# Kernel tuning notes

Hardware: AMD Instinct MI355X
Metric: run time of the kernel (lower is better)

## Reference

```python
import jax, jax.numpy as jnp
import numpy as np

WS = 8          # window size
HEAD_DIM = 32
C = 128
B, H, W = 8, 256, 256


def _grid_sample(img, grid):
    # torch F.grid_sample, bilinear, padding_mode='zeros', align_corners=True
    # img [N,C,Hi,Wi]; grid [N,Ho,Wo,2] with (x,y) in [-1,1]
    N, Cc, Hi, Wi = img.shape
    gx = (grid[..., 0] + 1.0) * 0.5 * (Wi - 1)
    gy = (grid[..., 1] + 1.0) * 0.5 * (Hi - 1)
    x0 = jnp.floor(gx); y0 = jnp.floor(gy)
    wx1 = gx - x0; wy1 = gy - y0

    def gather(ix, iy):
        valid = ((ix >= 0) & (ix < Wi) & (iy >= 0) & (iy < Hi)).astype(img.dtype)
        ixc = jnp.clip(ix, 0, Wi - 1).astype(jnp.int32)
        iyc = jnp.clip(iy, 0, Hi - 1).astype(jnp.int32)
        v = jax.vmap(lambda im, yy, xx: im[:, yy, xx])(img, iyc, ixc)  # [N,C,Ho,Wo]
        return v * valid[:, None]

    return (gather(x0, y0) * ((1 - wx1) * (1 - wy1))[:, None]
            + gather(x0 + 1, y0) * (wx1 * (1 - wy1))[:, None]
            + gather(x0, y0 + 1) * ((1 - wx1) * wy1)[:, None]
            + gather(x0 + 1, y0 + 1) * (wx1 * wy1)[:, None])


def _rel_bias(rpp):
    cord = np.array([[i, j] for i in range(WS) for j in range(WS)])
    rel = cord[:, None, :] - cord[None, :, :] + WS - 1   # [p2,p2,2]
    return rpp[:, rel[..., 0], rel[..., 1]]               # [h,p2,p2]


def _mask(w1, w2, p, shift):
    s = p - shift
    m = np.zeros((w1, w2, p, p, p, p), dtype=bool)
    m[-1, :, :s, :, s:, :] = True
    m[-1, :, s:, :, :s, :] = True
    m[:, -1, :, :s, :, s:] = True
    m[:, -1, :, s:, :, :s] = True
    return jnp.asarray(m.reshape(1, 1, w1 * w2, p * p, p * p))


def setup_inputs() -> dict:
    key = jax.random.key(0)
    ks = jax.random.split(key, 8)
    s = 0.02
    return {
        'x': jax.random.normal(ks[0], (B, H, W, C), jnp.float32),
        'rpp': jax.random.normal(ks[1], (C // HEAD_DIM, 2 * WS - 1, 2 * WS - 1), jnp.float32) * s,
        'wi_w': jax.random.normal(ks[2], (C, 2), jnp.float32) * s,
        'wi_b': jnp.zeros((2,), jnp.float32),
        'w1_w': jax.random.normal(ks[3], (C, 2), jnp.float32) * s,
        'w1_b': jnp.zeros((2,), jnp.float32),
        'w2_w': jax.random.normal(ks[4], (WS * WS * 2, 2), jnp.float32) * s,
        'w2_b': jnp.zeros((2,), jnp.float32),
        'q_w': jax.random.normal(ks[5], (C, C), jnp.float32) * s,
        'q_b': jnp.zeros((C,), jnp.float32),
        'kv_w': jax.random.normal(ks[6], (C, 2 * C), jnp.float32) * s,
        'kv_b': jnp.zeros((2 * C,), jnp.float32),
        'o_w': jax.random.normal(ks[7], (C, C), jnp.float32) * s,
        'o_b': jnp.zeros((C,), jnp.float32),
    }


def reference(x, rpp, wi_w, wi_b, w1_w, w1_b, w2_w, w2_b, q_w, q_b, kv_w, kv_b, o_w, o_b):
    shift = WS // 2
    b, Hh, Ww, c = x.shape
    w1, w2 = Hh // WS, Ww // WS
    nw, p2 = w1 * w2, WS * WS
    h = c // HEAD_DIM

    # cyclic shift (type != 'W')
    x = jnp.roll(x, (-shift, -shift), axis=(1, 2))
    xw = x.reshape(b, w1, WS, w2, WS, c).transpose(0, 1, 3, 2, 4, 5)  # [b,w1,w2,p,p,c]

    off_intra = xw @ wi_w + wi_b                                       # [b,w1,w2,p,p,2]
    oi = xw @ w1_w + w1_b                                              # [b,w1,w2,p,p,2]
    oi = oi.reshape(b, w1, w2, WS * WS * 2) @ w2_w + w2_b              # [b,w1,w2,2]

    # --- inter-window deformable sampling ---
    gy, gx = np.meshgrid(np.arange(w1), np.arange(w2), indexing='ij')
    gridw = jnp.asarray(np.stack((gx, gy), -1), jnp.float32)           # [w1,w2,2]
    og = gridw[None, :, :, None, None, :] + oi[:, :, :, None, None, :]
    og = jnp.broadcast_to(og, (b, w1, w2, WS, WS, 2))
    og = og / ((max(w1, w2) - 1) / 2) - 1.0
    ximg = xw.transpose(0, 3, 4, 5, 1, 2).reshape(b * p2, c, w1, w2)
    gint = og.transpose(0, 3, 4, 1, 2, 5).reshape(b * p2, w1, w2, 2)
    xd = _grid_sample(ximg, gint)                                      # [b*p2,c,w1,w2]
    xd = xd.reshape(b, WS, WS, c, w1, w2).transpose(0, 4, 5, 1, 2, 3)  # [b,w1,w2,p,p,c]

    # --- intra-window deformable sampling ---
    gy, gx = np.meshgrid(np.arange(WS), np.arange(WS), indexing='ij')
    gridp = jnp.asarray(np.stack((gx, gy), -1), jnp.float32)           # [p,p,2]
    og2 = gridp[None, None] + off_intra.reshape(b, nw, WS, WS, 2)
    og2 = og2 / ((WS - 1) / 2) - 1.0
    xd2 = xd.transpose(0, 1, 2, 5, 3, 4).reshape(b * nw, c, WS, WS)
    g2 = og2.reshape(b * nw, WS, WS, 2)
    xd2 = _grid_sample(xd2, g2).reshape(b, w1, w2, c, WS, WS).transpose(0, 1, 2, 4, 5, 3)

    # --- windowed attention ---
    xq = xw.reshape(b, nw, p2, c)
    xkv = xd2.reshape(b, nw, p2, c)
    q = (xq @ q_w + q_b).reshape(b, nw, p2, h, HEAD_DIM).transpose(3, 0, 1, 2, 4)
    kv = (xkv @ kv_w + kv_b).reshape(b, nw, p2, 2 * h, HEAD_DIM)
    k = kv[..., :h, :].transpose(3, 0, 1, 2, 4)
    v = kv[..., h:, :].transpose(3, 0, 1, 2, 4)

    scale = HEAD_DIM ** (-0.5)
    sim = jnp.einsum('hbwpc,hbwqc->hbwpq', q, k) * scale
    sim = sim + _rel_bias(rpp)[:, None, None]
    sim = jnp.where(_mask(w1, w2, WS, shift), -jnp.inf, sim)
    probs = jax.nn.softmax(sim, axis=-1)
    out = jnp.einsum('hbwpq,hbwqc->hbwpc', probs, v)
    out = out.transpose(1, 2, 3, 0, 4).reshape(b, nw, p2, c)
    out = out @ o_w + o_b
    out = out.reshape(b, w1, w2, WS, WS, c).transpose(0, 1, 3, 2, 4, 5).reshape(b, Hh, Ww, c)
    out = jnp.roll(out, (shift, shift), axis=(1, 2))
    return out
```

## Files before the change

### kernel.cpp

```cpp
#include <hip/hip_runtime.h>
#include <hip/hip_bf16.h>


#define WS_    8
#define SHIFT_ 4
#define C_     128
#define IMG_   256

typedef __attribute__((ext_vector_type(8))) short short8;
typedef __attribute__((ext_vector_type(4))) short short4v;
typedef __attribute__((ext_vector_type(4))) float f32x4;

#define MFMA(a,b,c) __builtin_amdgcn_mfma_f32_16x16x32_bf16((a),(b),(c),0,0,0)

__device__ __forceinline__ short f2bf(float f){
    unsigned u = __float_as_uint(f);
    u = u + 0x7fffu + ((u >> 16) & 1u);
    return (short)(u >> 16);
}
__device__ __forceinline__ float bf2f(short s){
    return __uint_as_float(((unsigned)(unsigned short)s) << 16);
}

__global__ void dgwa_prep(const float* __restrict__ q_w, const float* __restrict__ kv_w,
                          const float* __restrict__ o_w, short* __restrict__ ws){
    int idx = blockIdx.x*256 + threadIdx.x;
    if (idx < 16384){ int co = idx>>7, ci = idx&127; ws[idx] = f2bf(q_w[ci*128 + co]); }
    else if (idx < 49152){ int i = idx-16384; int co = i>>7, ci = i&127; ws[idx] = f2bf(kv_w[ci*256 + co]); }
    else { int i = idx-49152; int co = i>>7, ci = i&127; ws[idx] = f2bf(o_w[ci*128 + co]); }
}

__global__ __launch_bounds__(512, 4)
void dgwa_fused(const float* __restrict__ x, const float* __restrict__ rpp,
                const float* __restrict__ wi_w, const float* __restrict__ wi_b,
                const float* __restrict__ w1_w, const float* __restrict__ w1_b,
                const float* __restrict__ w2_w, const float* __restrict__ w2_b,
                const float* __restrict__ q_b,  const float* __restrict__ kv_b,
                const float* __restrict__ o_b,
                const short* __restrict__ wsw,
                float* __restrict__ out)
{
    __shared__ __align__(16) char smem[75296];
    short* s_xw   = (short*)(smem);
    short* s_xd2  = (short*)(smem + 17408);
    short* s_p    = (short*)(smem + 17408);
    float* s_outT = (float*)(smem + 17408);
    short* s_k    = (short*)(smem + 34816);
    short* s_xd   = (short*)(smem + 34816);
    short* s_vT   = (short*)(smem + 52224);
    float* s_rpp  = (float*)(smem + 70656);
    float* s_off  = (float*)(smem + 74256);
    float* s_red  = (float*)(smem + 74768);
    float* s_oi   = (float*)(smem + 75280);

    const int t   = threadIdx.x;
    const int wv  = t >> 6, l = t & 63, l15 = l & 15, quad = l >> 4;
    const int win = blockIdx.x;
    const int bb  = win >> 10, wy = (win >> 5) & 31, wx = win & 31;
    const f32x4 zf = {0.f, 0.f, 0.f, 0.f};

    const short* qw  = wsw;
    const short* kvw = wsw + 16384;
    const short* ow  = wsw + 49152;

    {
        const int tok = t >> 3, part = t & 7;
        const int i = tok >> 3, j = tok & 7;
        const int grow = (wy*8 + i + SHIFT_) & 255;
        const int gcol = (wx*8 + j + SHIFT_) & 255;
        const float* xr = x + (((size_t)bb*IMG_ + grow)*IMG_ + gcol)*C_ + part*16;
        float di0=0.f, di1=0.f, d10=0.f, d11=0.f;
        #pragma unroll
        for (int c4 = 0; c4 < 4; ++c4){
            const float4 a4 = *(const float4*)(xr + c4*4);
            const int ch = part*16 + c4*4;
            di0 += a4.x*wi_w[ch*2+0]+a4.y*wi_w[ch*2+2]+a4.z*wi_w[ch*2+4]+a4.w*wi_w[ch*2+6];
            di1 += a4.x*wi_w[ch*2+1]+a4.y*wi_w[ch*2+3]+a4.z*wi_w[ch*2+5]+a4.w*wi_w[ch*2+7];
            d10 += a4.x*w1_w[ch*2+0]+a4.y*w1_w[ch*2+2]+a4.z*w1_w[ch*2+4]+a4.w*w1_w[ch*2+6];
            d11 += a4.x*w1_w[ch*2+1]+a4.y*w1_w[ch*2+3]+a4.z*w1_w[ch*2+5]+a4.w*w1_w[ch*2+7];
            short4v sv = { f2bf(a4.x), f2bf(a4.y), f2bf(a4.z), f2bf(a4.w) };
            *(short4v*)&s_xw[tok*136 + part*16 + c4*4] = sv;
        }
        di0 += __shfl_xor(di0,1); di0 += __shfl_xor(di0,2); di0 += __shfl_xor(di0,4);
        di1 += __shfl_xor(di1,1); di1 += __shfl_xor(di1,2); di1 += __shfl_xor(di1,4);
        d10 += __shfl_xor(d10,1); d10 += __shfl_xor(d10,2); d10 += __shfl_xor(d10,4);
        d11 += __shfl_xor(d11,1); d11 += __shfl_xor(d11,2); d11 += __shfl_xor(d11,4);
        if (part == 0){
            s_off[tok*2+0] = di0 + wi_b[0];
            s_off[tok*2+1] = di1 + wi_b[1];
            s_red[tok*2+0] = d10 + w1_b[0];
            s_red[tok*2+1] = d11 + w1_b[1];
        }
    }
    for (int idx = t; idx < 900; idx += 512) s_rpp[idx] = rpp[idx];
    __syncthreads();
    if (t < 64){
        const float a0 = s_red[t*2+0], a1 = s_red[t*2+1];
        float p0 = a0*w2_w[(t*2+0)*2+0] + a1*w2_w[(t*2+1)*2+0];
        float p1 = a0*w2_w[(t*2+0)*2+1] + a1*w2_w[(t*2+1)*2+1];
        #pragma unroll
        for (int m = 1; m < 64; m <<= 1){ p0 += __shfl_xor(p0,m); p1 += __shfl_xor(p1,m); }
        if (t == 0){ s_oi[0] = p0 + w2_b[0]; s_oi[1] = p1 + w2_b[1]; }
    }
    __syncthreads();

    {
        const int tok = t >> 3, part = t & 7;
        const int i = tok >> 3, j = tok & 7;
        const float gx = (float)wx + s_oi[0];
        const float gy = (float)wy + s_oi[1];
        const float fx0 = floorf(gx), fy0 = floorf(gy);
        const int ix0 = (int)fx0, iy0 = (int)fy0;
        const float fx = gx - fx0, fy = gy - fy0;
        const float cw[4] = {(1.f-fx)*(1.f-fy), fx*(1.f-fy), (1.f-fx)*fy, fx*fy};
        float4 acc4[4];
        #pragma unroll
        for (int c4 = 0; c4 < 4; ++c4) acc4[c4] = make_float4(0.f,0.f,0.f,0.f);
        #pragma unroll
        for (int cc = 0; cc < 4; ++cc){
            const int cx = ix0 + (cc & 1), cy = iy0 + (cc >> 1);
            if (cx >= 0 && cx < 32 && cy >= 0 && cy < 32){
                const int rr = (cy*8 + i + SHIFT_) & 255;
                const int cl = (cx*8 + j + SHIFT_) & 255;
                const float* p = x + (((size_t)bb*IMG_ + rr)*IMG_ + cl)*C_ + part*16;
                const float w = cw[cc];
                #pragma unroll
                for (int c4 = 0; c4 < 4; ++c4){
                    const float4 v = *(const float4*)(p + c4*4);
                    acc4[c4].x += w*v.x; acc4[c4].y += w*v.y;
                    acc4[c4].z += w*v.z; acc4[c4].w += w*v.w;
                }
            }
        }
        #pragma unroll
        for (int c4 = 0; c4 < 4; ++c4){
            short4v sv = { f2bf(acc4[c4].x), f2bf(acc4[c4].y), f2bf(acc4[c4].z), f2bf(acc4[c4].w) };
            *(short4v*)&s_xd[tok*136 + part*16 + c4*4] = sv;
        }
    }
    __syncthreads();

    {
        const int tok = t >> 3, part = t & 7;
        const int i = tok >> 3, j = tok & 7;
        const float sx = (float)j + s_off[tok*2+0];
        const float sy = (float)i + s_off[tok*2+1];
        const float fx0 = floorf(sx), fy0 = floorf(sy);
        const int jx0 = (int)fx0, jy0 = (int)fy0;
        const float fx = sx - fx0, fy = sy - fy0;
        float4 acc4[4];
        #pragma unroll
        for (int c4 = 0; c4 < 4; ++c4) acc4[c4] = make_float4(0.f,0.f,0.f,0.f);
        #pragma unroll
        for (int cc = 0; cc < 4; ++cc){
            const int cx = jx0 + (cc & 1), cy = jy0 + (cc >> 1);
            const float w = ((cc & 1) ? fx : 1.f-fx) * ((cc >> 1) ? fy : 1.f-fy);
            if (cx >= 0 && cx < 8 && cy >= 0 && cy < 8){
                const short* p = &s_xd[(cy*8 + cx)*136 + part*16];
                #pragma unroll
                for (int c4 = 0; c4 < 4; ++c4){
                    const short4v sv = *(const short4v*)(p + c4*4);
                    acc4[c4].x += w*bf2f(sv.x); acc4[c4].y += w*bf2f(sv.y);
                    acc4[c4].z += w*bf2f(sv.z); acc4[c4].w += w*bf2f(sv.w);
                }
            }
        }
        #pragma unroll
        for (int c4 = 0; c4 < 4; ++c4){
            short4v sv = { f2bf(acc4[c4].x), f2bf(acc4[c4].y), f2bf(acc4[c4].z), f2bf(acc4[c4].w) };
            *(short4v*)&s_xd2[tok*136 + part*16 + c4*4] = sv;
        }
    }
    __syncthreads();

    {
        f32x4 acc[2][4];
        #pragma unroll
        for (int nn = 0; nn < 2; ++nn)
            #pragma unroll
            for (int mt = 0; mt < 4; ++mt) acc[nn][mt] = zf;
        #pragma unroll
        for (int ks = 0; ks < 4; ++ks){
            const int co = ks*32 + quad*8;
            const short8 b0 = *(const short8*)&kvw[(32*wv +      l15)*128 + co];
            const short8 b1 = *(const short8*)&kvw[(32*wv + 16 + l15)*128 + co];
            #pragma unroll
            for (int mt = 0; mt < 4; ++mt){
                const short8 a = *(const short8*)&s_xd2[(16*mt + l15)*136 + co];
                acc[0][mt] = MFMA(a, b0, acc[0][mt]);
                acc[1][mt] = MFMA(a, b1, acc[1][mt]);
            }
        }
        #pragma unroll
        for (int nn = 0; nn < 2; ++nn){
            const int col = 32*wv + 16*nn + l15;
            const float bias = kv_b[col];
            if (col < 128){
                #pragma unroll
                for (int mt = 0; mt < 4; ++mt)
                    #pragma unroll
                    for (int r = 0; r < 4; ++r){
                        const int tokr = 16*mt + 4*quad + r;
                        s_k[tokr*136 + col] = f2bf(acc[nn][mt][r] + bias);
                    }
            } else {
                const int vr = col - 128;
                #pragma unroll
                for (int mt = 0; mt < 4; ++mt)
                    #pragma unroll
                    for (int rp = 0; rp < 2; ++rp){
                        const int tokr = 16*mt + 4*quad + 2*rp;
                        const unsigned lo = (unsigned short)f2bf(acc[nn][mt][2*rp]   + bias);
                        const unsigned hi = (unsigned short)f2bf(acc[nn][mt][2*rp+1] + bias);
                        *(unsigned*)&s_vT[vr*72 + tokr] = lo | (hi << 16);
                    }
            }
        }
    }
    __syncthreads();

    {
        f32x4 qacc[4];
        #pragma unroll
        for (int mt = 0; mt < 4; ++mt) qacc[mt] = zf;
        #pragma unroll
        for (int ks = 0; ks < 4; ++ks){
            const int co = ks*32 + quad*8;
            const short8 b = *(const short8*)&qw[(16*wv + l15)*128 + co];
            #pragma unroll
            for (int mt = 0; mt < 4; ++mt){
                const short8 a = *(const short8*)&s_xw[(16*mt + l15)*136 + co];
                qacc[mt] = MFMA(a, b, qacc[mt]);
            }
        }
        __syncthreads();
        const int col = 16*wv + l15;
        const float bias = q_b[col];
        #pragma unroll
        for (int mt = 0; mt < 4; ++mt)
            #pragma unroll
            for (int r = 0; r < 4; ++r)
                s_xw[(16*mt + 4*quad + r)*136 + col] = f2bf(qacc[mt][r] + bias);
    }
    __syncthreads();

    short8 ka[4], bq[4];
    if (wv < 4){
        const int h = wv;
        #pragma unroll
        for (int mt = 0; mt < 4; ++mt)
            ka[mt] = *(const short8*)&s_k [(16*mt + l15)*136 + 32*h + quad*8];
        #pragma unroll
        for (int nt = 0; nt < 4; ++nt)
            bq[nt] = *(const short8*)&s_xw[(16*nt + l15)*136 + 32*h + quad*8];
    }
    __syncthreads();
    if (wv < 4){
        const int h = wv;
        const bool mrow = (wy == 31), mcol = (wx == 31);
        #pragma unroll
        for (int nt = 0; nt < 4; ++nt){
            f32x4 sc[4];
            #pragma unroll
            for (int mt = 0; mt < 4; ++mt)
                sc[mt] = MFMA(ka[mt], bq[nt], zf);
            const int qtok = 16*nt + l15;
            const int iq = qtok >> 3, jq = qtok & 7;
            float ssum = 0.f;
            #pragma unroll
            for (int mt = 0; mt < 4; ++mt){
                #pragma unroll
                for (int r = 0; r < 4; ++r){
                    const int ktok = 16*mt + 4*quad + r;
                    const int ik = ktok >> 3, jk = ktok & 7;
                    const float sv = sc[mt][r]*0.1767766952966369f
                                   + s_rpp[h*225 + (iq-ik+7)*15 + (jq-jk+7)];
                    const bool masked = (mrow && ((iq<4)!=(ik<4))) || (mcol && ((jq<4)!=(jk<4)));
                    const float e = masked ? 0.f : __expf(sv);
                    sc[mt][r] = e;
                    ssum += e;
                }
            }
            ssum += __shfl_xor(ssum, 16);
            ssum += __shfl_xor(ssum, 32);
            const float rs = 1.f / ssum;
            #pragma unroll
            for (int mt = 0; mt < 4; ++mt)
                #pragma unroll
                for (int rp = 0; rp < 2; ++rp){
                    const int ktok = 16*mt + 4*quad + 2*rp;
                    const unsigned lo = (unsigned short)f2bf(sc[mt][2*rp]   * rs);
                    const unsigned hi = (unsigned short)f2bf(sc[mt][2*rp+1] * rs);
                    *(unsigned*)&s_p[h*4352 + qtok*68 + ktok] = lo | (hi << 16);
                }
        }
    }
    __syncthreads();

    {
        const int h = wv >> 1, mh = wv & 1;
        short8 av[2];
        #pragma unroll
        for (int ks = 0; ks < 2; ++ks)
            av[ks] = *(const short8*)&s_vT[(32*h + 16*mh + l15)*72 + ks*32 + quad*8];
        f32x4 po[4];
        #pragma unroll
        for (int nt = 0; nt < 4; ++nt) po[nt] = zf;
        #pragma unroll
        for (int nt = 0; nt < 4; ++nt)
            #pragma unroll
            for (int ks = 0; ks < 2; ++ks){
                const short8 bp = *(const short8*)&s_p[h*4352 + (16*nt + l15)*68 + ks*32 + quad*8];
                po[nt] = MFMA(av[ks], bp, po[nt]);
            }
        #pragma unroll
        for (int nt = 0; nt < 4; ++nt){
            const int qtok = 16*nt + l15;
            #pragma unroll
            for (int rp = 0; rp < 2; ++rp){
                const int drow = 32*h + 16*mh + 4*quad + 2*rp;
                const unsigned lo = (unsigned short)f2bf(po[nt][2*rp]);
                const unsigned hi = (unsigned short)f2bf(po[nt][2*rp+1]);
                *(unsigned*)&s_xw[qtok*136 + drow] = lo | (hi << 16);
            }
        }
    }
    __syncthreads();

    {
        f32x4 oc[4];
        #pragma unroll
        for (int nt = 0; nt < 4; ++nt) oc[nt] = zf;
        #pragma unroll
        for (int ks = 0; ks < 4; ++ks){
            const int co = ks*32 + quad*8;
            const short8 aw = *(const short8*)&ow[(16*wv + l15)*128 + co];
            #pragma unroll
            for (int nt = 0; nt < 4; ++nt){
                const short8 bt = *(const short8*)&s_xw[(16*nt + l15)*136 + co];
                oc[nt] = MFMA(aw, bt, oc[nt]);
            }
        }
        const float4 ob = *(const float4*)&o_b[16*wv + 4*quad];
        const float obr[4] = {ob.x, ob.y, ob.z, ob.w};
        #pragma unroll
        for (int nt = 0; nt < 4; ++nt){
            const int tok = 16*nt + l15;
            #pragma unroll
            for (int r = 0; r < 4; ++r){
                const int cout = 16*wv + 4*quad + r;
                s_outT[cout*66 + tok] = oc[nt][r] + obr[r];
            }
        }
    }
    __syncthreads();

    {
        const int chan = t & 127;
        #pragma unroll
        for (int it = 0; it < 16; ++it){
            const int tok = (t >> 7) + it*4;
            const int i = tok >> 3, j = tok & 7;
            const int orow = (wy*8 + i + SHIFT_) & 255;
            const int ocol = (wx*8 + j + SHIFT_) & 255;
            out[(((size_t)bb*IMG_ + orow)*IMG_ + ocol)*C_ + chan] = s_outT[chan*66 + tok];
        }
    }
}

extern "C" void kernel_launch(void* const* d_in, const int* in_sizes, int n_in,
                              void* d_out, int out_size, void* d_ws, size_t ws_size,
                              hipStream_t stream) {
    (void)in_sizes; (void)n_in; (void)out_size; (void)ws_size;
    const float* x    = (const float*)d_in[0];
    const float* rpp  = (const float*)d_in[1];
    const float* wi_w = (const float*)d_in[2];
    const float* wi_b = (const float*)d_in[3];
    const float* w1_w = (const float*)d_in[4];
    const float* w1_b = (const float*)d_in[5];
    const float* w2_w = (const float*)d_in[6];
    const float* w2_b = (const float*)d_in[7];
    const float* q_w  = (const float*)d_in[8];
    const float* q_b  = (const float*)d_in[9];
    const float* kv_w = (const float*)d_in[10];
    const float* kv_b = (const float*)d_in[11];
    const float* o_w  = (const float*)d_in[12];
    const float* o_b  = (const float*)d_in[13];
    float* out = (float*)d_out;
    short* ws  = (short*)d_ws;

    dgwa_prep<<<dim3(256), dim3(256), 0, stream>>>(q_w, kv_w, o_w, ws);
    dgwa_fused<<<dim3(8192), dim3(512), 0, stream>>>(
        x, rpp, wi_w, wi_b, w1_w, w1_b, w2_w, w2_b,
        q_b, kv_b, o_b, ws, out);
}
```

Measured before the change: 765.8 us.

## Shrink LDS footprint and split attention into halves to raise occupancy

Reworks the shared-memory plan of the fused window-attention kernel to cut LDS from about 75KB to about 54KB. It does this by aliasing the K and V^T buffers, keeping per-token offsets and the window offset in registers instead of LDS, storing the relative-position bias as bf16, and processing the softmax/PV stage in two halves of query tiles so the probability buffer is half as large. The Q projection is reordered to run first, and launch bounds move from 4 to 6 waves per EU. The aim is to fit more blocks per CU and hide memory latency better. The costs are extra barriers, a tighter register budget that may cause spills, and bf16 rounding of the bias table.

```diff
diff --git a/kernel.cpp b/kernel.cpp
--- a/kernel.cpp
+++ b/kernel.cpp
@@ -30,7 +30,7 @@
     else { int i = idx-49152; int co = i>>7, ci = i&127; ws[idx] = f2bf(o_w[ci*128 + co]); }
 }
 
-__global__ __launch_bounds__(512, 4)
+__global__ __launch_bounds__(512, 6)
 void dgwa_fused(const float* __restrict__ x, const float* __restrict__ rpp,
                 const float* __restrict__ wi_w, const float* __restrict__ wi_b,
                 const float* __restrict__ w1_w, const float* __restrict__ w1_b,
@@ -40,18 +40,16 @@
                 const short* __restrict__ wsw,
                 float* __restrict__ out)
 {
-    __shared__ __align__(16) char smem[75296];
+    __shared__ __align__(16) char smem[54032];
     short* s_xw   = (short*)(smem);
+    float* s_red  = (float*)(smem + 17408);
     short* s_xd2  = (short*)(smem + 17408);
+    short* s_k    = (short*)(smem + 17408);
     short* s_p    = (short*)(smem + 17408);
     float* s_outT = (float*)(smem + 17408);
-    short* s_k    = (short*)(smem + 34816);
     short* s_xd   = (short*)(smem + 34816);
-    short* s_vT   = (short*)(smem + 52224);
-    float* s_rpp  = (float*)(smem + 70656);
-    float* s_off  = (float*)(smem + 74256);
-    float* s_red  = (float*)(smem + 74768);
-    float* s_oi   = (float*)(smem + 75280);
+    short* s_vT   = (short*)(smem + 34816);
+    short* s_rpp  = (short*)(smem + 52224);
 
     const int t   = threadIdx.x;
     const int wv  = t >> 6, l = t & 63, l15 = l & 15, quad = l >> 4;
@@ -62,6 +60,9 @@
     const short* qw  = wsw;
     const short* kvw = wsw + 16384;
     const short* ow  = wsw + 49152;
+
+    float off0, off1;
+    float oi0, oi1;
 
     {
         const int tok = t >> 3, part = t & 7;
@@ -85,30 +86,31 @@
         di1 += __shfl_xor(di1,1); di1 += __shfl_xor(di1,2); di1 += __shfl_xor(di1,4);
         d10 += __shfl_xor(d10,1); d10 += __shfl_xor(d10,2); d10 += __shfl_xor(d10,4);
         d11 += __shfl_xor(d11,1); d11 += __shfl_xor(d11,2); d11 += __shfl_xor(d11,4);
+        off0 = di0 + wi_b[0];
+        off1 = di1 + wi_b[1];
         if (part == 0){
-            s_off[tok*2+0] = di0 + wi_b[0];
-            s_off[tok*2+1] = di1 + wi_b[1];
             s_red[tok*2+0] = d10 + w1_b[0];
             s_red[tok*2+1] = d11 + w1_b[1];
         }
     }
-    for (int idx = t; idx < 900; idx += 512) s_rpp[idx] = rpp[idx];
-    __syncthreads();
-    if (t < 64){
-        const float a0 = s_red[t*2+0], a1 = s_red[t*2+1];
-        float p0 = a0*w2_w[(t*2+0)*2+0] + a1*w2_w[(t*2+1)*2+0];
-        float p1 = a0*w2_w[(t*2+0)*2+1] + a1*w2_w[(t*2+1)*2+1];
+    for (int idx = t; idx < 900; idx += 512) s_rpp[idx] = f2bf(rpp[idx]);
+    __syncthreads();
+
+    {
+        const float a0 = s_red[l*2+0], a1 = s_red[l*2+1];
+        float p0 = a0*w2_w[(l*2+0)*2+0] + a1*w2_w[(l*2+1)*2+0];
+        float p1 = a0*w2_w[(l*2+0)*2+1] + a1*w2_w[(l*2+1)*2+1];
         #pragma unroll
         for (int m = 1; m < 64; m <<= 1){ p0 += __shfl_xor(p0,m); p1 += __shfl_xor(p1,m); }
-        if (t == 0){ s_oi[0] = p0 + w2_b[0]; s_oi[1] = p1 + w2_b[1]; }
-    }
-    __syncthreads();
+        oi0 = p0 + w2_b[0];
+        oi1 = p1 + w2_b[1];
+    }
 
     {
         const int tok = t >> 3, part = t & 7;
         const int i = tok >> 3, j = tok & 7;
-        const float gx = (float)wx + s_oi[0];
-        const float gy = (float)wy + s_oi[1];
+        const float gx = (float)wx + oi0;
+        const float gy = (float)wy + oi1;
         const float fx0 = floorf(gx), fy0 = floorf(gy);
         const int ix0 = (int)fx0, iy0 = (int)fy0;
         const float fx = gx - fx0, fy = gy - fy0;
@@ -143,8 +145,8 @@
     {
         const int tok = t >> 3, part = t & 7;
         const int i = tok >> 3, j = tok & 7;
-        const float sx = (float)j + s_off[tok*2+0];
-        const float sy = (float)i + s_off[tok*2+1];
+        const float sx = (float)j + off0;
+        const float sy = (float)i + off1;
         const float fx0 = floorf(sx), fy0 = floorf(sy);
         const int jx0 = (int)fx0, jy0 = (int)fy0;
         const float fx = sx - fx0, fy = sy - fy0;
@@ -173,8 +175,34 @@
     }
     __syncthreads();
 
-    {
-        f32x4 acc[2][4];
+    f32x4 qacc[4];
+    {
+        #pragma unroll
+        for (int mt = 0; mt < 4; ++mt) qacc[mt] = zf;
+        #pragma unroll
+        for (int ks = 0; ks < 4; ++ks){
+            const int co = ks*32 + quad*8;
+            const short8 b = *(const short8*)&qw[(16*wv + l15)*128 + co];
+            #pragma unroll
+            for (int mt = 0; mt < 4; ++mt){
+                const short8 a = *(const short8*)&s_xw[(16*mt + l15)*136 + co];
+                qacc[mt] = MFMA(a, b, qacc[mt]);
+            }
+        }
+    }
+    __syncthreads();
+
+    {
+        const int col = 16*wv + l15;
+        const float bias = q_b[col];
+        #pragma unroll
+        for (int mt = 0; mt < 4; ++mt)
+            #pragma unroll
+            for (int r = 0; r < 4; ++r)
+                s_xw[(16*mt + 4*quad + r)*136 + col] = f2bf(qacc[mt][r] + bias);
+    }
+    f32x4 acc[2][4];
+    {
         #pragma unroll
         for (int nn = 0; nn < 2; ++nn)
             #pragma unroll
@@ -191,20 +219,11 @@
                 acc[1][mt] = MFMA(a, b1, acc[1][mt]);
             }
         }
-        #pragma unroll
-        for (int nn = 0; nn < 2; ++nn){
-            const int col = 32*wv + 16*nn + l15;
-            const float bias = kv_b[col];
-            if (col < 128){
-                #pragma unroll
-                for (int mt = 0; mt < 4; ++mt)
-                    #pragma unroll
-                    for (int r = 0; r < 4; ++r){
-                        const int tokr = 16*mt + 4*quad + r;
-                        s_k[tokr*136 + col] = f2bf(acc[nn][mt][r] + bias);
-                    }
-            } else {
-                const int vr = col - 128;
+        if (wv >= 4){
+            #pragma unroll
+            for (int nn = 0; nn < 2; ++nn){
+                const int vr = 32*(wv-4) + 16*nn + l15;
+                const float bias = kv_b[128 + vr];
                 #pragma unroll
                 for (int mt = 0; mt < 4; ++mt)
                     #pragma unroll
@@ -212,120 +231,112 @@
                         const int tokr = 16*mt + 4*quad + 2*rp;
                         const unsigned lo = (unsigned short)f2bf(acc[nn][mt][2*rp]   + bias);
                         const unsigned hi = (unsigned short)f2bf(acc[nn][mt][2*rp+1] + bias);
-                        *(unsigned*)&s_vT[vr*72 + tokr] = lo | (hi << 16);
+                        *(unsigned*)&s_vT[vr*68 + tokr] = lo | (hi << 16);
                     }
             }
         }
     }
     __syncthreads();
-
-    {
-        f32x4 qacc[4];
-        #pragma unroll
-        for (int mt = 0; mt < 4; ++mt) qacc[mt] = zf;
-        #pragma unroll
-        for (int ks = 0; ks < 4; ++ks){
-            const int co = ks*32 + quad*8;
-            const short8 b = *(const short8*)&qw[(16*wv + l15)*128 + co];
-            #pragma unroll
-            for (int mt = 0; mt < 4; ++mt){
-                const short8 a = *(const short8*)&s_xw[(16*mt + l15)*136 + co];
-                qacc[mt] = MFMA(a, b, qacc[mt]);
-            }
-        }
-        __syncthreads();
-        const int col = 16*wv + l15;
-        const float bias = q_b[col];
-        #pragma unroll
-        for (int mt = 0; mt < 4; ++mt)
-            #pragma unroll
-            for (int r = 0; r < 4; ++r)
-                s_xw[(16*mt + 4*quad + r)*136 + col] = f2bf(qacc[mt][r] + bias);
-    }
-    __syncthreads();
-
-    short8 ka[4], bq[4];
+    if (wv < 4){
+        #pragma unroll
+        for (int nn = 0; nn < 2; ++nn){
+            const int col = 32*wv + 16*nn + l15;
+            const float bias = kv_b[col];
+            #pragma unroll
+            for (int mt = 0; mt < 4; ++mt)
+                #pragma unroll
+                for (int r = 0; r < 4; ++r){
+                    const int tokr = 16*mt + 4*quad + r;
+                    s_k[tokr*136 + col] = f2bf(acc[nn][mt][r] + bias);
+                }
+        }
+    }
+    __syncthreads();
+
+    short8 ka[4];
     if (wv < 4){
         const int h = wv;
         #pragma unroll
         for (int mt = 0; mt < 4; ++mt)
-            ka[mt] = *(const short8*)&s_k [(16*mt + l15)*136 + 32*h + quad*8];
-        #pragma unroll
-        for (int nt = 0; nt < 4; ++nt)
-            bq[nt] = *(const short8*)&s_xw[(16*nt + l15)*136 + 32*h + quad*8];
-    }
-    __syncthreads();
-    if (wv < 4){
-        const int h = wv;
-        const bool mrow = (wy == 31), mcol = (wx == 31);
-        #pragma unroll
-        for (int nt = 0; nt < 4; ++nt){
-            f32x4 sc[4];
-            #pragma unroll
-            for (int mt = 0; mt < 4; ++mt)
-                sc[mt] = MFMA(ka[mt], bq[nt], zf);
-            const int qtok = 16*nt + l15;
-            const int iq = qtok >> 3, jq = qtok & 7;
-            float ssum = 0.f;
-            #pragma unroll
-            for (int mt = 0; mt < 4; ++mt){
-                #pragma unroll
-                for (int r = 0; r < 4; ++r){
-                    const int ktok = 16*mt + 4*quad + r;
-                    const int ik = ktok >> 3, jk = ktok & 7;
-                    const float sv = sc[mt][r]*0.1767766952966369f
-                                   + s_rpp[h*225 + (iq-ik+7)*15 + (jq-jk+7)];
-                    const bool masked = (mrow && ((iq<4)!=(ik<4))) || (mcol && ((jq<4)!=(jk<4)));
-                    const float e = masked ? 0.f : __expf(sv);
-                    sc[mt][r] = e;
-                    ssum += e;
-                }
-            }
-            ssum += __shfl_xor(ssum, 16);
-            ssum += __shfl_xor(ssum, 32);
-            const float rs = 1.f / ssum;
-            #pragma unroll
-            for (int mt = 0; mt < 4; ++mt)
+            ka[mt] = *(const short8*)&s_k[(16*mt + l15)*136 + 32*h + quad*8];
+    }
+    short8 av[2];
+    {
+        const int vrow = 32*(wv >> 1) + 16*(wv & 1) + l15;
+        #pragma unroll
+        for (int ks = 0; ks < 2; ++ks)
+            av[ks] = *(const short8*)&s_vT[vrow*68 + ks*32 + quad*8];
+    }
+    __syncthreads();
+
+    #pragma unroll
+    for (int hf = 0; hf < 2; ++hf){
+        if (wv < 4){
+            const int h = wv;
+            const bool mrow = (wy == 31), mcol = (wx == 31);
+            #pragma unroll
+            for (int ntl = 0; ntl < 2; ++ntl){
+                const int nt = 2*hf + ntl;
+                const short8 bq = *(const short8*)&s_xw[(16*nt + l15)*136 + 32*h + quad*8];
+                f32x4 sc[4];
+                #pragma unroll
+                for (int mt = 0; mt < 4; ++mt)
+                    sc[mt] = MFMA(ka[mt], bq, zf);
+                const int qtok = 16*nt + l15;
+                const int iq = qtok >> 3, jq = qtok & 7;
+                float ssum = 0.f;
+                #pragma unroll
+                for (int mt = 0; mt < 4; ++mt){
+                    #pragma unroll
+                    for (int r = 0; r < 4; ++r){
+                        const int ktok = 16*mt + 4*quad + r;
+                        const int ik = ktok >> 3, jk = ktok & 7;
+                        const float sv = sc[mt][r]*0.1767766952966369f
+                                       + bf2f(s_rpp[h*225 + (iq-ik+7)*15 + (jq-jk+7)]);
+                        const bool masked = (mrow && ((iq<4)!=(ik<4))) || (mcol && ((jq<4)!=(jk<4)));
+                        const float e = masked ? 0.f : __expf(sv);
+                        sc[mt][r] = e;
+                        ssum += e;
+                    }
+                }
+                ssum += __shfl_xor(ssum, 16);
+                ssum += __shfl_xor(ssum, 32);
+                const float rs = 1.f / ssum;
+                #pragma unroll
+                for (int mt = 0; mt < 4; ++mt)
+                    #pragma unroll
+                    for (int rp = 0; rp < 2; ++rp){
+                        const int ktok = 16*mt + 4*quad + 2*rp;
+                        const unsigned lo = (unsigned short)f2bf(sc[mt][2*rp]   * rs);
+                        const unsigned hi = (unsigned short)f2bf(sc[mt][2*rp+1] * rs);
+                        *(unsigned*)&s_p[h*2176 + (16*ntl + l15)*68 + ktok] = lo | (hi << 16);
+                    }
+            }
+        }
+        __syncthreads();
+
+        {
+            const int h = wv >> 1, mh = wv & 1;
+            #pragma unroll
+            for (int ntl = 0; ntl < 2; ++ntl){
+                f32x4 po = zf;
+                #pragma unroll
+                for (int ks = 0; ks < 2; ++ks){
+                    const short8 bp = *(const short8*)&s_p[h*2176 + (16*ntl + l15)*68 + ks*32 + quad*8];
+                    po = MFMA(av[ks], bp, po);
+                }
+                const int qtok = 32*hf + 16*ntl + l15;
                 #pragma unroll
                 for (int rp = 0; rp < 2; ++rp){
-                    const int ktok = 16*mt + 4*quad + 2*rp;
-                    const unsigned lo = (unsigned short)f2bf(sc[mt][2*rp]   * rs);
-                    const unsigned hi = (unsigned short)f2bf(sc[mt][2*rp+1] * rs);
-                    *(unsigned*)&s_p[h*4352 + qtok*68 + ktok] = lo | (hi << 16);
-                }
-        }
-    }
-    __syncthreads();
-
-    {
-        const int h = wv >> 1, mh = wv & 1;
-        short8 av[2];
-        #pragma unroll
-        for (int ks = 0; ks < 2; ++ks)
-            av[ks] = *(const short8*)&s_vT[(32*h + 16*mh + l15)*72 + ks*32 + quad*8];
-        f32x4 po[4];
-        #pragma unroll
-        for (int nt = 0; nt < 4; ++nt) po[nt] = zf;
-        #pragma unroll
-        for (int nt = 0; nt < 4; ++nt)
-            #pragma unroll
-            for (int ks = 0; ks < 2; ++ks){
-                const short8 bp = *(const short8*)&s_p[h*4352 + (16*nt + l15)*68 + ks*32 + quad*8];
-                po[nt] = MFMA(av[ks], bp, po[nt]);
-            }
-        #pragma unroll
-        for (int nt = 0; nt < 4; ++nt){
-            const int qtok = 16*nt + l15;
-            #pragma unroll
-            for (int rp = 0; rp < 2; ++rp){
-                const int drow = 32*h + 16*mh + 4*quad + 2*rp;
-                const unsigned lo = (unsigned short)f2bf(po[nt][2*rp]);
-                const unsigned hi = (unsigned short)f2bf(po[nt][2*rp+1]);
-                *(unsigned*)&s_xw[qtok*136 + drow] = lo | (hi << 16);
-            }
-        }
-    }
-    __syncthreads();
+                    const int drow = 32*h + 16*mh + 4*quad + 2*rp;
+                    const unsigned lo = (unsigned short)f2bf(po[2*rp]);
+                    const unsigned hi = (unsigned short)f2bf(po[2*rp+1]);
+                    *(unsigned*)&s_xw[qtok*136 + drow] = lo | (hi << 16);
+                }
+            }
+        }
+        __syncthreads();
+    }
 
     {
         f32x4 oc[4];
```

Measured after the change: 802.4 us. +4.8%, slower.
